# Kernel tuning notes

Measured on AMD Instinct MI355X. Metric: run time of the kernel, lower is better.

Reference implementation:

```python
import jax, jax.numpy as jnp
import numpy as np

N = 300000
MAX_TORSION = 7
MAX_RIGID = 8
MAX_SS = 3
MAX_ATOM = 24
NRES = 22
EPS = 1e-6


def v_norm_safe(v):
    # normalize last dim with epsilon clamp (torch v_norm_safe analogue)
    return v / jnp.clip(jnp.linalg.norm(v, axis=-1, keepdims=True), EPS)


def combine_operations(X, Y):
    # X, Y: [..., 4, 3] rigid ops (3x3 rotation rows + 1 translation row)
    rot = X[..., :3, :] @ Y[..., :3, :]
    t = jnp.einsum('...ij,...j->...i', X[..., :3, :], Y[..., 3, :]) + X[..., 3, :]
    return jnp.concatenate([rot, t[..., None, :]], axis=-2)


def setup_inputs() -> dict:
    key = jax.random.key(0)
    ks = jax.random.split(key, 9)
    return {
        'output_0': jax.random.normal(ks[0], (N, 2 * MAX_TORSION + MAX_SS, 1), jnp.float32),
        'output_1': jax.random.normal(ks[1], (N, 3, 3), jnp.float32),
        'pos': jax.random.normal(ks[2], (N, 3), jnp.float32),
        'ss': jax.random.randint(ks[3], (N,), 0, MAX_SS),
        'residue_type': jax.random.randint(ks[4], (N,), 0, NRES),
        'rigid_transforms': jax.random.normal(ks[5], (MAX_SS, NRES, MAX_RIGID, 4, 3), jnp.float32),
        'rigid_groups': jax.random.normal(ks[6], (MAX_SS, NRES, MAX_ATOM, 3), jnp.float32),
        'transforms_dep': jax.random.randint(ks[7], (NRES, MAX_RIGID), 0, MAX_RIGID),
        'rigids_dep': jax.random.randint(ks[8], (NRES, MAX_ATOM), 0, MAX_RIGID),
    }


def reference(output_0, output_1, pos, ss, residue_type,
              rigid_transforms, rigid_groups, transforms_dep, rigids_dep):
    # ---- StructureModule.output_to_opr_6D ----
    bb0 = output_1[:, :2]                                   # [N,2,3]
    e0 = v_norm_safe(bb0[:, 0])
    v1 = bb0[:, 1]
    u1 = v1 - e0 * jnp.sum(e0 * v1, axis=-1, keepdims=True)
    e1 = v_norm_safe(u1)
    e2 = jnp.cross(e0, e1)
    rot = jnp.stack([e0, e1, e2], axis=1).swapaxes(-1, -2)  # [N,3,3]
    t = 0.1 * output_1[:, 2][:, None, :]                    # [N,1,3]
    bb = jnp.concatenate([rot, t], axis=1)                  # [N,4,3]
    sc = v_norm_safe(output_0[:, :2 * MAX_TORSION].reshape(-1, MAX_TORSION, 2))

    # ---- build_structure ----
    transforms = rigid_transforms[ss, residue_type]         # [N,8,4,3]
    rigids = rigid_groups[ss, residue_type]                 # [N,24,3]
    tdep = transforms_dep[residue_type]                     # [N,8]
    rdep = rigids_dep[residue_type]                         # [N,24]

    n = output_0.shape[0]
    c, s = sc[..., 0], sc[..., 1]                           # [N,7]
    zr = jnp.zeros_like(c)
    on = jnp.ones_like(c)
    tor_rot = jnp.stack([
        jnp.stack([on, zr, zr], axis=-1),
        jnp.stack([zr, c, -s], axis=-1),
        jnp.stack([zr, s, c], axis=-1),
    ], axis=-2)                                             # [N,7,3,3]
    tor = jnp.concatenate(
        [tor_rot, jnp.zeros((n, MAX_TORSION, 1, 3), output_0.dtype)], axis=2)
    opr0 = jnp.concatenate([bb[:, :3], (bb[:, 3] + pos)[:, None]], axis=1)  # [N,4,3]
    opr = jnp.concatenate([opr0[:, None], tor], axis=1)     # [N,8,4,3]

    opr = combine_operations(transforms, opr)
    for i_tor in range(1, MAX_RIGID):                       # fixed 7-step dependency chain
        prev = jnp.take_along_axis(opr, tdep[:, i_tor][:, None, None, None], axis=1)[:, 0]
        opr = opr.at[:, i_tor].set(combine_operations(prev, opr[:, i_tor]))

    opr_g = jnp.take_along_axis(opr, rdep[:, :, None, None], axis=1)  # [N,24,4,3]
    R = jnp.einsum('naij,naj->nai', opr_g[:, :, :3], rigids) + opr_g[:, :, 3]
    return (R, opr[:, 0])
```

## Files before the change

### kernel.cpp

```cpp
#include <hip/hip_runtime.h>
#include <math.h>

#define NRES 22

#define ST_F    0
#define SG_F    6600
#define STD_I   11616
#define SRD_I   11814
#define TBL_F   12364
#define CHUNK_F 1856
#define SMEM_BYTES ((TBL_F + 4 * CHUNK_F) * 4)

__device__ __forceinline__ void sel8(const float (&fr)[8][12], int d, float (&P)[12]) {
    const bool b0 = (d & 1) != 0;
    const bool b1 = (d & 2) != 0;
    const bool b2 = (d & 4) != 0;
#pragma unroll
    for (int k = 0; k < 12; ++k) {
        float a01 = b0 ? fr[1][k] : fr[0][k];
        float a23 = b0 ? fr[3][k] : fr[2][k];
        float a45 = b0 ? fr[5][k] : fr[4][k];
        float a67 = b0 ? fr[7][k] : fr[6][k];
        float b03 = b1 ? a23 : a01;
        float b47 = b1 ? a67 : a45;
        P[k] = b2 ? b47 : b03;
    }
}

__device__ __forceinline__ void apply_point(const float (&F)[12], float x, float y, float z,
                                            float &px, float &py, float &pz) {
    px = fmaf(F[0], x, fmaf(F[1], y, fmaf(F[2], z, F[9])));
    py = fmaf(F[3], x, fmaf(F[4], y, fmaf(F[5], z, F[10])));
    pz = fmaf(F[6], x, fmaf(F[7], y, fmaf(F[8], z, F[11])));
}

__device__ __forceinline__ void wave_stage(const float* __restrict__ src, float* dst,
                                           int nF, int lane) {
    const int n4 = nF >> 2;
    const float4* s4 = (const float4*)src;
    float4* d4 = (float4*)dst;
    for (int i = lane; i < n4; i += 64) d4[i] = s4[i];
    const int rem = nF & 3;
    if (lane < rem) {
        const int b = n4 << 2;
        dst[b + lane] = src[b + lane];
    }
}

extern "C" __global__ __launch_bounds__(256, 2)
void model_kernel(const float* __restrict__ o0,
                  const float* __restrict__ o1,
                  const float* __restrict__ pos,
                  const int*   __restrict__ ssArr,
                  const int*   __restrict__ rtArr,
                  const float* __restrict__ rigT,
                  const float* __restrict__ rigG,
                  const int*   __restrict__ tdepArr,
                  const int*   __restrict__ rdepArr,
                  float* __restrict__ outR,
                  float* __restrict__ outF,
                  int N)
{
    extern __shared__ __align__(16) float smem[];
    int* smemI = (int*)smem;
    const int tid  = threadIdx.x;
    const int lane = tid & 63;
    const int wave = tid >> 6;

    {
        const float4* s4 = (const float4*)rigT;
        for (int t = tid; t < 1584; t += 256) {
            float4 v = s4[t];
            int rec = t / 24;
            int k   = (t - rec * 24) << 2;
            *(float4*)(smem + ST_F + rec * 100 + k) = v;
        }
    }
    {
        const float4* s4 = (const float4*)rigG;
        for (int t = tid; t < 1188; t += 256) {
            float4 v = s4[t];
            int rec = t / 18;
            int k   = (t - rec * 18) << 2;
            *(float4*)(smem + SG_F + rec * 76 + k) = v;
        }
    }
    for (int t = tid; t < 176; t += 256)
        smemI[STD_I + (t >> 3) * 9 + (t & 7)] = tdepArr[t];
    for (int t = tid; t < 528; t += 256) {
        int r = t / 24;
        smemI[SRD_I + r * 25 + (t - r * 24)] = rdepArr[t];
    }
    __syncthreads();

    float* chunk = smem + TBL_F + wave * CHUNK_F;
    const int gstride = (int)gridDim.x * 256;

    for (int base = (int)blockIdx.x * 256; base < N; base += gstride) {
        const int wres0 = base + wave * 64;
        const int cnt   = min(64, N - wres0);

        asm volatile("s_waitcnt lgkmcnt(0)" ::: "memory");

        if (cnt > 0) {
            wave_stage(o0  + (size_t)wres0 * 17, chunk,        cnt * 17, lane);
            wave_stage(o1  + (size_t)wres0 * 9,  chunk + 1088, cnt * 9,  lane);
            wave_stage(pos + (size_t)wres0 * 3,  chunk + 1664, cnt * 3,  lane);
        }
        asm volatile("s_waitcnt lgkmcnt(0)" ::: "memory");

        const int  res   = wres0 + lane;
        const bool alive = (lane < cnt);

        float  fr[8][12];
        float4 out4[18];

        if (alive) {
            const int s    = ssArr[res];
            const int rt   = rtArr[res];
            const int sr22 = s * NRES + rt;

            const float* myo0 = chunk + lane * 17;
            float c[7], sn[7];
#pragma unroll
            for (int t = 0; t < 7; ++t) {
                float cr = myo0[2 * t], sr = myo0[2 * t + 1];
                float inv = rsqrtf(fmaxf(cr * cr + sr * sr, 1e-12f));
                c[t]  = cr * inv;
                sn[t] = sr * inv;
            }

            const float* myo1 = chunk + 1088 + lane * 9;
            float r0x = myo1[0], r0y = myo1[1], r0z = myo1[2];
            float v1x = myo1[3], v1y = myo1[4], v1z = myo1[5];
            float t2x = myo1[6], t2y = myo1[7], t2z = myo1[8];
            float inv0 = rsqrtf(fmaxf(r0x * r0x + r0y * r0y + r0z * r0z, 1e-12f));
            float e0x = r0x * inv0, e0y = r0y * inv0, e0z = r0z * inv0;
            float d01 = e0x * v1x + e0y * v1y + e0z * v1z;
            float u1x = v1x - e0x * d01, u1y = v1y - e0y * d01, u1z = v1z - e0z * d01;
            float inv1 = rsqrtf(fmaxf(u1x * u1x + u1y * u1y + u1z * u1z, 1e-12f));
            float e1x = u1x * inv1, e1y = u1y * inv1, e1z = u1z * inv1;
            float e2x = e0y * e1z - e0z * e1y;
            float e2y = e0z * e1x - e0x * e1z;
            float e2z = e0x * e1y - e0y * e1x;
            const float* myp = chunk + 1664 + lane * 3;
            float btx = 0.1f * t2x + myp[0];
            float bty = 0.1f * t2y + myp[1];
            float btz = 0.1f * t2z + myp[2];

            const float4* T4 = (const float4*)smem + sr22 * 25;

            {
                float4 q0 = T4[0], q1 = T4[1], q2 = T4[2];
                float T0[12] = {q0.x, q0.y, q0.z, q0.w, q1.x, q1.y, q1.z, q1.w,
                                q2.x, q2.y, q2.z, q2.w};
#pragma unroll
                for (int i = 0; i < 3; ++i) {
                    float a = T0[i * 3 + 0], b = T0[i * 3 + 1], d = T0[i * 3 + 2];
                    fr[0][i * 3 + 0] = a * e0x + b * e0y + d * e0z;
                    fr[0][i * 3 + 1] = a * e1x + b * e1y + d * e1z;
                    fr[0][i * 3 + 2] = a * e2x + b * e2y + d * e2z;
                    fr[0][9 + i]     = a * btx + b * bty + d * btz + T0[9 + i];
                }
            }

#pragma unroll
            for (int f = 1; f < 8; ++f) {
                float4 q0 = T4[f * 3 + 0], q1 = T4[f * 3 + 1], q2 = T4[f * 3 + 2];
                float Tf[12] = {q0.x, q0.y, q0.z, q0.w, q1.x, q1.y, q1.z, q1.w,
                                q2.x, q2.y, q2.z, q2.w};
                float cc = c[f - 1], ssn = sn[f - 1];
#pragma unroll
                for (int i = 0; i < 3; ++i) {
                    fr[f][i * 3 + 0] = Tf[i * 3 + 0];
                    fr[f][i * 3 + 1] = Tf[i * 3 + 1] * cc + Tf[i * 3 + 2] * ssn;
                    fr[f][i * 3 + 2] = Tf[i * 3 + 2] * cc - Tf[i * 3 + 1] * ssn;
                    fr[f][9 + i]     = Tf[9 + i];
                }
            }

            const int* tdp = smemI + STD_I + rt * 9;
#pragma unroll
            for (int i = 1; i < 8; ++i) {
                float P[12];
                sel8(fr, tdp[i] & 7, P);
                float Y[12];
#pragma unroll
                for (int k = 0; k < 12; ++k) Y[k] = fr[i][k];
#pragma unroll
                for (int r = 0; r < 3; ++r) {
                    float a = P[r * 3 + 0], b = P[r * 3 + 1], d = P[r * 3 + 2];
#pragma unroll
                    for (int j = 0; j < 3; ++j)
                        fr[i][r * 3 + j] = a * Y[j] + b * Y[3 + j] + d * Y[6 + j];
                    fr[i][9 + r] = a * Y[9] + b * Y[10] + d * Y[11] + P[9 + r];
                }
            }

            float4* OF4 = (float4*)outF + (size_t)res * 3;
            OF4[0] = make_float4(fr[0][0], fr[0][1], fr[0][2], fr[0][3]);
            OF4[1] = make_float4(fr[0][4], fr[0][5], fr[0][6], fr[0][7]);
            OF4[2] = make_float4(fr[0][8], fr[0][9], fr[0][10], fr[0][11]);

            const float4* G4  = (const float4*)smem + 1650 + sr22 * 19;
            const int*    rdp = smemI + SRD_I + rt * 25;
#pragma unroll
            for (int ck = 0; ck < 6; ++ck) {
                int d0 = rdp[ck * 4 + 0] & 7, d1 = rdp[ck * 4 + 1] & 7;
                int d2 = rdp[ck * 4 + 2] & 7, d3 = rdp[ck * 4 + 3] & 7;
                float4 g0 = G4[ck * 3 + 0], g1 = G4[ck * 3 + 1], g2 = G4[ck * 3 + 2];
                float P[12];
                float p0x, p0y, p0z, p1x, p1y, p1z, p2x, p2y, p2z, p3x, p3y, p3z;
                sel8(fr, d0, P); apply_point(P, g0.x, g0.y, g0.z, p0x, p0y, p0z);
                sel8(fr, d1, P); apply_point(P, g0.w, g1.x, g1.y, p1x, p1y, p1z);
                sel8(fr, d2, P); apply_point(P, g1.z, g1.w, g2.x, p2x, p2y, p2z);
                sel8(fr, d3, P); apply_point(P, g2.y, g2.z, g2.w, p3x, p3y, p3z);
                out4[ck * 3 + 0] = make_float4(p0x, p0y, p0z, p1x);
                out4[ck * 3 + 1] = make_float4(p1y, p1z, p2x, p2y);
                out4[ck * 3 + 2] = make_float4(p2z, p3x, p3y, p3z);
            }
        }

#pragma unroll 1
        for (int r = 0; r < 4; ++r) {
            const int rb = wres0 + r * 16;
            const int vr = min(16, N - rb);
            if (vr > 0) {
                asm volatile("s_waitcnt lgkmcnt(0)" ::: "memory");
                if ((lane >> 4) == r && (lane & 15) < vr) {
                    float4* slotp = (float4*)(chunk + (lane & 15) * 76);
#pragma unroll
                    for (int j = 0; j < 18; ++j) slotp[j] = out4[j];
                }
                asm volatile("s_waitcnt lgkmcnt(0)" ::: "memory");
                const float4* c4  = (const float4*)chunk;
                float4*       dst = (float4*)outR + (size_t)rb * 18;
                const int     n4r = vr * 18;
                for (int i = lane; i < n4r; i += 64) {
                    int slot = i / 18;
                    dst[i] = c4[slot * 19 + (i - slot * 18)];
                }
            }
        }
    }
}

extern "C" void kernel_launch(void* const* d_in, const int* in_sizes, int n_in,
                              void* d_out, int out_size, void* d_ws, size_t ws_size,
                              hipStream_t stream) {
    const float* o0   = (const float*)d_in[0];
    const float* o1   = (const float*)d_in[1];
    const float* pos  = (const float*)d_in[2];
    const int*   ssA  = (const int*)d_in[3];
    const int*   rtA  = (const int*)d_in[4];
    const float* rigT = (const float*)d_in[5];
    const float* rigG = (const float*)d_in[6];
    const int*   tdep = (const int*)d_in[7];
    const int*   rdep = (const int*)d_in[8];

    const int N = in_sizes[3];
    float* outR = (float*)d_out;
    float* outF = (float*)d_out + (size_t)N * 72;

    static bool attr_set = false;
    if (!attr_set) {
        hipFuncSetAttribute((const void*)model_kernel,
                            hipFuncAttributeMaxDynamicSharedMemorySize, SMEM_BYTES);
        attr_set = true;
    }

    int grid = (N + 255) / 256;
    if (grid > 512) grid = 512;
    model_kernel<<<grid, 256, SMEM_BYTES, stream>>>(o0, o1, pos, ssA, rtA, rigT, rigG,
                                                    tdep, rdep, outR, outF, N);
}
```

Baseline: 182.7 us.

## Split atom placement across two lanes per residue via LDS frame exchange

The rigid transform and group tables are no longer staged into LDS and are read directly from global memory (L2-cached). Each residue's eight composed frames are written to a swizzled per-wave LDS region, and the 24-atom placement is split between two half-waves, with each lane computing 12 atoms by reading frames from LDS instead of running register-based sel8 selects. This removes the select-heavy register work and the large per-lane output array, which should lower register pressure, at the cost of more LDS traffic and waitcnt barriers. The grid cap is raised from 512 to 768 blocks.

```diff
diff --git a/kernel.cpp b/kernel.cpp
--- a/kernel.cpp
+++ b/kernel.cpp
@@ -3,13 +3,11 @@
 
 #define NRES 22
 
-#define ST_F    0
-#define SG_F    6600
-#define STD_I   11616
-#define SRD_I   11814
-#define TBL_F   12364
-#define CHUNK_F 1856
-#define SMEM_BYTES ((TBL_F + 4 * CHUNK_F) * 4)
+#define TDEP_I 0
+#define RDEP_I 198
+#define WREG_F 752
+#define WREG_STRIDE 3072
+#define SMEM_BYTES ((WREG_F + 4 * WREG_STRIDE) * 4)
 
 __device__ __forceinline__ void sel8(const float (&fr)[8][12], int d, float (&P)[12]) {
     const bool b0 = (d & 1) != 0;
@@ -27,11 +25,14 @@
     }
 }
 
-__device__ __forceinline__ void apply_point(const float (&F)[12], float x, float y, float z,
-                                            float &px, float &py, float &pz) {
-    px = fmaf(F[0], x, fmaf(F[1], y, fmaf(F[2], z, F[9])));
-    py = fmaf(F[3], x, fmaf(F[4], y, fmaf(F[5], z, F[10])));
-    pz = fmaf(F[6], x, fmaf(F[7], y, fmaf(F[8], z, F[11])));
+__device__ __forceinline__ float4 frow(const float4* fbase, int s, int d, int j) {
+    int x = 3 * d + j;
+    int xs = (x & 24) | ((x ^ s) & 7);
+    return fbase[xs];
+}
+
+__device__ __forceinline__ float ap(float4 r, float x, float y, float z) {
+    return fmaf(r.x, x, fmaf(r.y, y, fmaf(r.z, z, r.w)));
 }
 
 __device__ __forceinline__ void wave_stage(const float* __restrict__ src, float* dst,
@@ -46,6 +47,8 @@
         dst[b + lane] = src[b + lane];
     }
 }
+
+#define LGKM0() asm volatile("s_waitcnt lgkmcnt(0)" ::: "memory")
 
 extern "C" __global__ __launch_bounds__(256, 2)
 void model_kernel(const float* __restrict__ o0,
@@ -67,60 +70,41 @@
     const int lane = tid & 63;
     const int wave = tid >> 6;
 
-    {
-        const float4* s4 = (const float4*)rigT;
-        for (int t = tid; t < 1584; t += 256) {
-            float4 v = s4[t];
-            int rec = t / 24;
-            int k   = (t - rec * 24) << 2;
-            *(float4*)(smem + ST_F + rec * 100 + k) = v;
-        }
-    }
-    {
-        const float4* s4 = (const float4*)rigG;
-        for (int t = tid; t < 1188; t += 256) {
-            float4 v = s4[t];
-            int rec = t / 18;
-            int k   = (t - rec * 18) << 2;
-            *(float4*)(smem + SG_F + rec * 76 + k) = v;
-        }
-    }
     for (int t = tid; t < 176; t += 256)
-        smemI[STD_I + (t >> 3) * 9 + (t & 7)] = tdepArr[t];
+        smemI[TDEP_I + (t >> 3) * 9 + (t & 7)] = tdepArr[t];
     for (int t = tid; t < 528; t += 256) {
         int r = t / 24;
-        smemI[SRD_I + r * 25 + (t - r * 24)] = rdepArr[t];
+        smemI[RDEP_I + r * 25 + (t - r * 24)] = rdepArr[t];
     }
     __syncthreads();
 
-    float* chunk = smem + TBL_F + wave * CHUNK_F;
+    float*  wreg  = smem + WREG_F + wave * WREG_STRIDE;
+    float4* wreg4 = (float4*)wreg;
     const int gstride = (int)gridDim.x * 256;
 
     for (int base = (int)blockIdx.x * 256; base < N; base += gstride) {
         const int wres0 = base + wave * 64;
         const int cnt   = min(64, N - wres0);
 
-        asm volatile("s_waitcnt lgkmcnt(0)" ::: "memory");
-
+        LGKM0();
         if (cnt > 0) {
-            wave_stage(o0  + (size_t)wres0 * 17, chunk,        cnt * 17, lane);
-            wave_stage(o1  + (size_t)wres0 * 9,  chunk + 1088, cnt * 9,  lane);
-            wave_stage(pos + (size_t)wres0 * 3,  chunk + 1664, cnt * 3,  lane);
+            wave_stage(o0  + (size_t)wres0 * 17, wreg,        cnt * 17, lane);
+            wave_stage(o1  + (size_t)wres0 * 9,  wreg + 1088, cnt * 9,  lane);
+            wave_stage(pos + (size_t)wres0 * 3,  wreg + 1664, cnt * 3,  lane);
         }
-        asm volatile("s_waitcnt lgkmcnt(0)" ::: "memory");
+        LGKM0();
 
         const int  res   = wres0 + lane;
         const bool alive = (lane < cnt);
 
-        float  fr[8][12];
-        float4 out4[18];
+        float fr[8][12];
 
         if (alive) {
             const int s    = ssArr[res];
             const int rt   = rtArr[res];
             const int sr22 = s * NRES + rt;
 
-            const float* myo0 = chunk + lane * 17;
+            const float* myo0 = wreg + lane * 17;
             float c[7], sn[7];
 #pragma unroll
             for (int t = 0; t < 7; ++t) {
@@ -130,7 +114,7 @@
                 sn[t] = sr * inv;
             }
 
-            const float* myo1 = chunk + 1088 + lane * 9;
+            const float* myo1 = wreg + 1088 + lane * 9;
             float r0x = myo1[0], r0y = myo1[1], r0z = myo1[2];
             float v1x = myo1[3], v1y = myo1[4], v1z = myo1[5];
             float t2x = myo1[6], t2y = myo1[7], t2z = myo1[8];
@@ -143,12 +127,12 @@
             float e2x = e0y * e1z - e0z * e1y;
             float e2y = e0z * e1x - e0x * e1z;
             float e2z = e0x * e1y - e0y * e1x;
-            const float* myp = chunk + 1664 + lane * 3;
+            const float* myp = wreg + 1664 + lane * 3;
             float btx = 0.1f * t2x + myp[0];
             float bty = 0.1f * t2y + myp[1];
             float btz = 0.1f * t2z + myp[2];
 
-            const float4* T4 = (const float4*)smem + sr22 * 25;
+            const float4* T4 = (const float4*)rigT + (size_t)sr22 * 24;
 
             {
                 float4 q0 = T4[0], q1 = T4[1], q2 = T4[2];
@@ -163,7 +147,6 @@
                     fr[0][9 + i]     = a * btx + b * bty + d * btz + T0[9 + i];
                 }
             }
-
 #pragma unroll
             for (int f = 1; f < 8; ++f) {
                 float4 q0 = T4[f * 3 + 0], q1 = T4[f * 3 + 1], q2 = T4[f * 3 + 2];
@@ -179,7 +162,7 @@
                 }
             }
 
-            const int* tdp = smemI + STD_I + rt * 9;
+            const int* tdp = smemI + TDEP_I + rt * 9;
 #pragma unroll
             for (int i = 1; i < 8; ++i) {
                 float P[12];
@@ -201,44 +184,83 @@
             OF4[0] = make_float4(fr[0][0], fr[0][1], fr[0][2], fr[0][3]);
             OF4[1] = make_float4(fr[0][4], fr[0][5], fr[0][6], fr[0][7]);
             OF4[2] = make_float4(fr[0][8], fr[0][9], fr[0][10], fr[0][11]);
-
-            const float4* G4  = (const float4*)smem + 1650 + sr22 * 19;
-            const int*    rdp = smemI + SRD_I + rt * 25;
-#pragma unroll
-            for (int ck = 0; ck < 6; ++ck) {
-                int d0 = rdp[ck * 4 + 0] & 7, d1 = rdp[ck * 4 + 1] & 7;
-                int d2 = rdp[ck * 4 + 2] & 7, d3 = rdp[ck * 4 + 3] & 7;
-                float4 g0 = G4[ck * 3 + 0], g1 = G4[ck * 3 + 1], g2 = G4[ck * 3 + 2];
-                float P[12];
-                float p0x, p0y, p0z, p1x, p1y, p1z, p2x, p2y, p2z, p3x, p3y, p3z;
-                sel8(fr, d0, P); apply_point(P, g0.x, g0.y, g0.z, p0x, p0y, p0z);
-                sel8(fr, d1, P); apply_point(P, g0.w, g1.x, g1.y, p1x, p1y, p1z);
-                sel8(fr, d2, P); apply_point(P, g1.z, g1.w, g2.x, p2x, p2y, p2z);
-                sel8(fr, d3, P); apply_point(P, g2.y, g2.z, g2.w, p3x, p3y, p3z);
-                out4[ck * 3 + 0] = make_float4(p0x, p0y, p0z, p1x);
-                out4[ck * 3 + 1] = make_float4(p1y, p1z, p2x, p2y);
-                out4[ck * 3 + 2] = make_float4(p2z, p3x, p3y, p3z);
-            }
         }
 
 #pragma unroll 1
-        for (int r = 0; r < 4; ++r) {
-            const int rb = wres0 + r * 16;
-            const int vr = min(16, N - rb);
-            if (vr > 0) {
-                asm volatile("s_waitcnt lgkmcnt(0)" ::: "memory");
-                if ((lane >> 4) == r && (lane & 15) < vr) {
-                    float4* slotp = (float4*)(chunk + (lane & 15) * 76);
-#pragma unroll
-                    for (int j = 0; j < 18; ++j) slotp[j] = out4[j];
-                }
-                asm volatile("s_waitcnt lgkmcnt(0)" ::: "memory");
-                const float4* c4  = (const float4*)chunk;
-                float4*       dst = (float4*)outR + (size_t)rb * 18;
-                const int     n4r = vr * 18;
-                for (int i = lane; i < n4r; i += 64) {
-                    int slot = i / 18;
-                    dst[i] = c4[slot * 19 + (i - slot * 18)];
+        for (int b = 0; b < 2; ++b) {
+            const int sb0  = wres0 + 32 * b;
+            const int scnt = min(32, cnt - 32 * b);
+            if (scnt <= 0) break;
+
+            const int  s32    = lane & 31;
+            const int  half   = lane >> 5;
+            const bool aalive = (s32 < scnt);
+
+            int rtp = 0, sr22p = 0;
+            float4 g[9];
+            if (aalive) {
+                const int resp = sb0 + s32;
+                rtp   = rtArr[resp];
+                sr22p = ssArr[resp] * NRES + rtp;
+                const float4* G4 = (const float4*)rigG + (size_t)sr22p * 18 + half * 9;
+#pragma unroll
+                for (int j = 0; j < 9; ++j) g[j] = G4[j];
+            }
+
+            LGKM0();
+            if (half == b && s32 < scnt) {
+                float4* fp = wreg4 + s32 * 24;
+#pragma unroll
+                for (int f = 0; f < 8; ++f)
+#pragma unroll
+                    for (int j = 0; j < 3; ++j) {
+                        int x  = f * 3 + j;
+                        int xs = (x & 24) | ((x ^ s32) & 7);
+                        fp[xs] = make_float4(fr[f][3 * j], fr[f][3 * j + 1],
+                                             fr[f][3 * j + 2], fr[f][9 + j]);
+                    }
+            }
+            LGKM0();
+
+            float4 outv[9];
+            if (aalive) {
+                const int*    rdp   = smemI + RDEP_I + rtp * 25 + half * 12;
+                const float4* fbase = wreg4 + s32 * 24;
+#pragma unroll
+                for (int ck = 0; ck < 3; ++ck) {
+                    int d0 = rdp[ck * 4 + 0] & 7, d1 = rdp[ck * 4 + 1] & 7;
+                    int d2 = rdp[ck * 4 + 2] & 7, d3 = rdp[ck * 4 + 3] & 7;
+                    float4 g0 = g[ck * 3 + 0], g1 = g[ck * 3 + 1], g2 = g[ck * 3 + 2];
+                    float4 r0, r1, r2;
+                    float p0x, p0y, p0z, p1x, p1y, p1z, p2x, p2y, p2z, p3x, p3y, p3z;
+                    r0 = frow(fbase, s32, d0, 0); r1 = frow(fbase, s32, d0, 1); r2 = frow(fbase, s32, d0, 2);
+                    p0x = ap(r0, g0.x, g0.y, g0.z); p0y = ap(r1, g0.x, g0.y, g0.z); p0z = ap(r2, g0.x, g0.y, g0.z);
+                    r0 = frow(fbase, s32, d1, 0); r1 = frow(fbase, s32, d1, 1); r2 = frow(fbase, s32, d1, 2);
+                    p1x = ap(r0, g0.w, g1.x, g1.y); p1y = ap(r1, g0.w, g1.x, g1.y); p1z = ap(r2, g0.w, g1.x, g1.y);
+                    r0 = frow(fbase, s32, d2, 0); r1 = frow(fbase, s32, d2, 1); r2 = frow(fbase, s32, d2, 2);
+                    p2x = ap(r0, g1.z, g1.w, g2.x); p2y = ap(r1, g1.z, g1.w, g2.x); p2z = ap(r2, g1.z, g1.w, g2.x);
+                    r0 = frow(fbase, s32, d3, 0); r1 = frow(fbase, s32, d3, 1); r2 = frow(fbase, s32, d3, 2);
+                    p3x = ap(r0, g2.y, g2.z, g2.w); p3y = ap(r1, g2.y, g2.z, g2.w); p3z = ap(r2, g2.y, g2.z, g2.w);
+                    outv[ck * 3 + 0] = make_float4(p0x, p0y, p0z, p1x);
+                    outv[ck * 3 + 1] = make_float4(p1y, p1z, p2x, p2y);
+                    outv[ck * 3 + 2] = make_float4(p2z, p3x, p3y, p3z);
+                }
+            }
+
+            LGKM0();
+            if (aalive) {
+                float4* hp = wreg4 + (s32 * 2 + half) * 11;
+#pragma unroll
+                for (int j = 0; j < 9; ++j) hp[j] = outv[j];
+            }
+            LGKM0();
+
+            {
+                float4*   dst = (float4*)outR + (size_t)sb0 * 18;
+                const int n4  = scnt * 18;
+                for (int i = lane; i < n4; i += 64) {
+                    int h = i / 9;
+                    dst[i] = wreg4[h * 11 + (i - h * 9)];
                 }
             }
         }
@@ -270,7 +292,7 @@
     }
 
     int grid = (N + 255) / 256;
-    if (grid > 512) grid = 512;
+    if (grid > 768) grid = 768;
     model_kernel<<<grid, 256, SMEM_BYTES, stream>>>(o0, o1, pos, ssA, rtA, rigT, rigG,
                                                     tdep, rdep, outR, outF, N);
 }
```

After: 264.1 us. 44.5% more time.

## Read rigid tables from global memory instead of LDS to raise occupancy

Applied to the files above, without the earlier changes.

Stops staging the rigid transform and group tables into shared memory and reads them straight from global (cached) memory. This shrinks LDS per block a lot, so the launch bound is raised to 4 blocks per CU and the grid is no longer capped at 512, giving one block per 256 residues. The intent is to cut the per-block table staging cost and to allow more resident waves. The cost is that each thread's table loads are now scattered global/L2 accesses rather than LDS reads, and the tighter register budget for 4 blocks per CU may cause spills given the large per-thread arrays.

```diff
diff --git a/kernel.cpp b/kernel.cpp
--- a/kernel.cpp
+++ b/kernel.cpp
@@ -3,13 +3,11 @@
 
 #define NRES 22
 
-#define ST_F    0
-#define SG_F    6600
-#define STD_I   11616
-#define SRD_I   11814
-#define TBL_F   12364
+#define TDEP_I 0
+#define RDEP_I 198
+#define WREG_F 752
 #define CHUNK_F 1856
-#define SMEM_BYTES ((TBL_F + 4 * CHUNK_F) * 4)
+#define SMEM_BYTES ((WREG_F + 4 * CHUNK_F) * 4)
 
 __device__ __forceinline__ void sel8(const float (&fr)[8][12], int d, float (&P)[12]) {
     const bool b0 = (d & 1) != 0;
@@ -47,7 +45,9 @@
     }
 }
 
-extern "C" __global__ __launch_bounds__(256, 2)
+#define LGKM0() asm volatile("s_waitcnt lgkmcnt(0)" ::: "memory")
+
+extern "C" __global__ __launch_bounds__(256, 4)
 void model_kernel(const float* __restrict__ o0,
                   const float* __restrict__ o1,
                   const float* __restrict__ pos,
@@ -67,47 +67,28 @@
     const int lane = tid & 63;
     const int wave = tid >> 6;
 
-    {
-        const float4* s4 = (const float4*)rigT;
-        for (int t = tid; t < 1584; t += 256) {
-            float4 v = s4[t];
-            int rec = t / 24;
-            int k   = (t - rec * 24) << 2;
-            *(float4*)(smem + ST_F + rec * 100 + k) = v;
-        }
-    }
-    {
-        const float4* s4 = (const float4*)rigG;
-        for (int t = tid; t < 1188; t += 256) {
-            float4 v = s4[t];
-            int rec = t / 18;
-            int k   = (t - rec * 18) << 2;
-            *(float4*)(smem + SG_F + rec * 76 + k) = v;
-        }
-    }
     for (int t = tid; t < 176; t += 256)
-        smemI[STD_I + (t >> 3) * 9 + (t & 7)] = tdepArr[t];
+        smemI[TDEP_I + (t >> 3) * 9 + (t & 7)] = tdepArr[t];
     for (int t = tid; t < 528; t += 256) {
         int r = t / 24;
-        smemI[SRD_I + r * 25 + (t - r * 24)] = rdepArr[t];
+        smemI[RDEP_I + r * 25 + (t - r * 24)] = rdepArr[t];
     }
     __syncthreads();
 
-    float* chunk = smem + TBL_F + wave * CHUNK_F;
+    float*  chunk  = smem + WREG_F + wave * CHUNK_F;
     const int gstride = (int)gridDim.x * 256;
 
     for (int base = (int)blockIdx.x * 256; base < N; base += gstride) {
         const int wres0 = base + wave * 64;
         const int cnt   = min(64, N - wres0);
 
-        asm volatile("s_waitcnt lgkmcnt(0)" ::: "memory");
-
+        LGKM0();
         if (cnt > 0) {
             wave_stage(o0  + (size_t)wres0 * 17, chunk,        cnt * 17, lane);
             wave_stage(o1  + (size_t)wres0 * 9,  chunk + 1088, cnt * 9,  lane);
             wave_stage(pos + (size_t)wres0 * 3,  chunk + 1664, cnt * 3,  lane);
         }
-        asm volatile("s_waitcnt lgkmcnt(0)" ::: "memory");
+        LGKM0();
 
         const int  res   = wres0 + lane;
         const bool alive = (lane < cnt);
@@ -148,7 +129,7 @@
             float bty = 0.1f * t2y + myp[1];
             float btz = 0.1f * t2z + myp[2];
 
-            const float4* T4 = (const float4*)smem + sr22 * 25;
+            const float4* T4 = (const float4*)rigT + (size_t)sr22 * 24;
 
             {
                 float4 q0 = T4[0], q1 = T4[1], q2 = T4[2];
@@ -163,7 +144,6 @@
                     fr[0][9 + i]     = a * btx + b * bty + d * btz + T0[9 + i];
                 }
             }
-
 #pragma unroll
             for (int f = 1; f < 8; ++f) {
                 float4 q0 = T4[f * 3 + 0], q1 = T4[f * 3 + 1], q2 = T4[f * 3 + 2];
@@ -179,7 +159,7 @@
                 }
             }
 
-            const int* tdp = smemI + STD_I + rt * 9;
+            const int* tdp = smemI + TDEP_I + rt * 9;
 #pragma unroll
             for (int i = 1; i < 8; ++i) {
                 float P[12];
@@ -202,8 +182,8 @@
             OF4[1] = make_float4(fr[0][4], fr[0][5], fr[0][6], fr[0][7]);
             OF4[2] = make_float4(fr[0][8], fr[0][9], fr[0][10], fr[0][11]);
 
-            const float4* G4  = (const float4*)smem + 1650 + sr22 * 19;
-            const int*    rdp = smemI + SRD_I + rt * 25;
+            const float4* G4  = (const float4*)rigG + (size_t)sr22 * 18;
+            const int*    rdp = smemI + RDEP_I + rt * 25;
 #pragma unroll
             for (int ck = 0; ck < 6; ++ck) {
                 int d0 = rdp[ck * 4 + 0] & 7, d1 = rdp[ck * 4 + 1] & 7;
@@ -226,13 +206,13 @@
             const int rb = wres0 + r * 16;
             const int vr = min(16, N - rb);
             if (vr > 0) {
-                asm volatile("s_waitcnt lgkmcnt(0)" ::: "memory");
+                LGKM0();
                 if ((lane >> 4) == r && (lane & 15) < vr) {
                     float4* slotp = (float4*)(chunk + (lane & 15) * 76);
 #pragma unroll
                     for (int j = 0; j < 18; ++j) slotp[j] = out4[j];
                 }
-                asm volatile("s_waitcnt lgkmcnt(0)" ::: "memory");
+                LGKM0();
                 const float4* c4  = (const float4*)chunk;
                 float4*       dst = (float4*)outR + (size_t)rb * 18;
                 const int     n4r = vr * 18;
@@ -269,8 +249,7 @@
         attr_set = true;
     }
 
-    int grid = (N + 255) / 256;
-    if (grid > 512) grid = 512;
+    const int grid = (N + 255) / 256;
     model_kernel<<<grid, 256, SMEM_BYTES, stream>>>(o0, o1, pos, ssA, rtA, rigT, rigG,
                                                     tdep, rdep, outR, outF, N);
 }
```

After: 329.4 us. 80.3% more time.
